# Kernel optimization log

Measured on AMD Instinct MI355X. Metric: run time of the kernel, lower is better.

Reference implementation:

```python
import jax, jax.numpy as jnp
import numpy as np

N_NODES = 100000
N_EDGES = 1600000
N_GRAPHS = 64
IN_C, HID, OUT_C = 9, 128, 2


def setup_inputs() -> dict:
    key = jax.random.key(0)
    ks = jax.random.split(key, 10)
    x = jax.random.normal(ks[0], (N_NODES, IN_C), dtype=jnp.float32)
    edge_index = jax.random.randint(ks[1], (2, N_EDGES), 0, N_NODES, dtype=jnp.int64)
    batch = jnp.sort(jax.random.randint(ks[2], (N_NODES,), 0, N_GRAPHS, dtype=jnp.int64))
    # GCNConv params (glorot-ish scale) and biases
    W1 = jax.random.normal(ks[3], (IN_C, HID), dtype=jnp.float32) / np.sqrt(IN_C)
    b1 = jnp.zeros((HID,), dtype=jnp.float32)
    W2 = jax.random.normal(ks[4], (HID, HID), dtype=jnp.float32) / np.sqrt(HID)
    b2 = jnp.zeros((HID,), dtype=jnp.float32)
    Wc = jax.random.normal(ks[5], (HID, OUT_C), dtype=jnp.float32) / np.sqrt(HID)
    bc = jnp.zeros((OUT_C,), dtype=jnp.float32)
    return {"x": x, "edge_index": edge_index, "batch": batch,
            "W1": W1, "b1": b1, "W2": W2, "b2": b2, "Wc": Wc, "bc": bc}


def _gcn_conv(x, row, col, dinv, W, b):
    # x: [N, Fin] -> [N, Fout]; symmetric-normalized scatter-add over edges+self-loops
    xw = x @ W                                   # dense GEMM
    norm = dinv[row] * dinv[col]                 # [E+N]
    msg = xw[row] * norm[:, None]                # gather + scale
    out = jax.ops.segment_sum(msg, col, num_segments=x.shape[0])  # scatter-add at target
    return out + b


def reference(x, edge_index, batch, W1, b1, W2, b2, Wc, bc):
    n = x.shape[0]
    loops = jnp.arange(n, dtype=edge_index.dtype)
    row = jnp.concatenate([edge_index[0], loops])  # sources (with self-loops)
    col = jnp.concatenate([edge_index[1], loops])  # targets
    deg = jax.ops.segment_sum(jnp.ones_like(col, dtype=x.dtype), col, num_segments=n)
    dinv = jnp.where(deg > 0, jax.lax.rsqrt(deg), 0.0)
    h = jax.nn.relu(_gcn_conv(x, row, col, dinv, W1, b1))
    h = jax.nn.relu(_gcn_conv(h, row, col, dinv, W2, b2))
    # global mean pool over graphs
    sums = jax.ops.segment_sum(h, batch, num_segments=N_GRAPHS)
    cnts = jax.ops.segment_sum(jnp.ones((n,), dtype=h.dtype), batch, num_segments=N_GRAPHS)
    pooled = sums / jnp.maximum(cnts, 1.0)[:, None]
    return pooled @ Wc + bc
```

## Files before the change

### kernel.cpp

```cpp
#include <hip/hip_runtime.h>

#define NN 100000
#define NE 1600000
#define NG 64
#define HIDC 128
#define INC 9
#define OUTC 2
#define BSH 9
#define NBK ((NN + 511) / 512)
#define EPB 4096
#define NBLKA ((NE + EPB - 1) / EPB)
#define CAP 12288

typedef unsigned int u32;

#define PACK_REC(lc, r) (((u32)(lc) << 17) | (u32)(r))
#define REC_LC(v) ((v) >> 17)
#define REC_ROW(v) ((v) & 0x1FFFFu)

__device__ inline float bf_lo(u32 u) { return __uint_as_float(u << 16); }
__device__ inline float bf_hi(u32 u) { return __uint_as_float(u & 0xFFFF0000u); }
__device__ inline u32 f2bf(float x) {
    u32 u = __float_as_uint(x);
    return (u + 0x7FFFu + ((u >> 16) & 1u)) >> 16;
}
__device__ inline u32 packbf(float a, float b) { return f2bf(a) | (f2bf(b) << 16); }

__global__ void k_zero196(int* bcnt) {
    int t = threadIdx.x;
    if (t < NBK) bcnt[t] = 0;
}

__global__ __launch_bounds__(256) void k_bscatter2(const int* __restrict__ row,
                                                   const int* __restrict__ col,
                                                   int* bcnt, u32* __restrict__ staging) {
    __shared__ u32 srec[EPB];
    __shared__ u32 sbkt[EPB];
    __shared__ int hist[NBK];
    __shared__ int base[NBK];
    int t = threadIdx.x;
    long e0 = (long)blockIdx.x * EPB;
    int n = (NE - e0 < EPB) ? (int)(NE - e0) : EPB;
    for (int i = t; i < n; i += 256) {
        u32 c = col[e0 + i];
        u32 r = row[e0 + i];
        srec[i] = PACK_REC(c & 511u, r);
        sbkt[i] = c >> BSH;
    }
    if (t < NBK) hist[t] = 0;
    __syncthreads();
    for (int i = t; i < n; i += 256) atomicAdd(&hist[sbkt[i]], 1);
    __syncthreads();
    if (t < NBK) {
        int h = hist[t];
        base[t] = h ? atomicAdd(&bcnt[t], h) : 0;
        hist[t] = 0;
    }
    __syncthreads();
    for (int i = t; i < n; i += 256) {
        int b = sbkt[i];
        int p = atomicAdd(&hist[b], 1) + base[b];
        if (p < CAP) staging[(long)b * CAP + p] = srec[i];
    }
}

__global__ __launch_bounds__(256) void k_bscan(const int* __restrict__ bcnt,
                                               int* __restrict__ bbase,
                                               int* __restrict__ offsets) {
    __shared__ int lds[256];
    int t = threadIdx.x;
    int v = (t < NBK) ? bcnt[t] : 0;
    lds[t] = v;
    __syncthreads();
    for (int d = 1; d < 256; d <<= 1) {
        int u = (t >= d) ? lds[t - d] : 0;
        __syncthreads();
        lds[t] += u;
        __syncthreads();
    }
    if (t < NBK) bbase[t] = lds[t] - v;
    if (t == 0) offsets[NN] = NE;
}

__global__ __launch_bounds__(256) void k_bcsr(const u32* __restrict__ staging,
                                              const int* __restrict__ bcnt,
                                              const int* __restrict__ bbase,
                                              int* __restrict__ offsets,
                                              float* __restrict__ dinv,
                                              int* __restrict__ csr_src) {
    __shared__ int cnt[512];
    __shared__ int cur[512];
    __shared__ int sc[256];
    int b = blockIdx.x, t = threadIdx.x;
    int nb0 = b << BSH;
    int nodes = NN - nb0 < 512 ? NN - nb0 : 512;
    int ne_b = bcnt[b];
    long s0b = (long)b * CAP;
    int e0 = bbase[b];
    cnt[t] = 0;
    cnt[t + 256] = 0;
    __syncthreads();
    for (int e = t; e < ne_b; e += 256)
        atomicAdd(&cnt[REC_LC(staging[s0b + e])], 1);
    __syncthreads();
    int c0 = cnt[2 * t], c1 = cnt[2 * t + 1];
    int s = c0 + c1;
    sc[t] = s;
    __syncthreads();
    for (int d = 1; d < 256; d <<= 1) {
        int u = (t >= d) ? sc[t - d] : 0;
        __syncthreads();
        sc[t] += u;
        __syncthreads();
    }
    int ex = sc[t] - s;
    cur[2 * t] = ex;
    cur[2 * t + 1] = ex + c0;
    if (2 * t < nodes) {
        offsets[nb0 + 2 * t] = e0 + ex;
        dinv[nb0 + 2 * t] = rsqrtf((float)(c0 + 1));
    }
    if (2 * t + 1 < nodes) {
        offsets[nb0 + 2 * t + 1] = e0 + ex + c0;
        dinv[nb0 + 2 * t + 1] = rsqrtf((float)(c1 + 1));
    }
    __syncthreads();
    for (int e = t; e < ne_b; e += 256) {
        u32 r = staging[s0b + e];
        int p = atomicAdd(&cur[REC_LC(r)], 1);
        csr_src[e0 + p] = (int)REC_ROW(r);
    }
}

__global__ __launch_bounds__(256) void k_xw1(const float* __restrict__ x,
                                             const float* __restrict__ W1,
                                             const float* __restrict__ dinv,
                                             u32* __restrict__ Ap2) {
    int tid = threadIdx.x;
    int i = blockIdx.x * 4 + (tid >> 6);
    int j = tid & 63;
    if (i >= NN) return;
    float acc0 = 0.f, acc1 = 0.f;
#pragma unroll
    for (int k = 0; k < INC; ++k) {
        float xv = x[i * INC + k];
        acc0 += xv * W1[k * HIDC + 2 * j];
        acc1 += xv * W1[k * HIDC + 2 * j + 1];
    }
    float di = dinv[i];
    Ap2[(long)i * 64 + j] = packbf(acc0 * di, acc1 * di);
}

__global__ __launch_bounds__(256) void k_gather(const u32* __restrict__ Ap2,
                                                const int* __restrict__ csr_src,
                                                const int* __restrict__ offsets,
                                                const float* __restrict__ dinv,
                                                u32* __restrict__ B2) {
    int i = (blockIdx.x * 256 + threadIdx.x) >> 6;
    if (i >= NN) return;
    int lane = threadIdx.x & 63;
    long base = (long)i * 64 + lane;
    u32 a = Ap2[base];
    float acc0 = bf_lo(a), acc1 = bf_hi(a);
    int beg = offsets[i], end = offsets[i + 1];
    int e = beg;
    for (; e + 8 <= end; e += 8) {
        int s0 = csr_src[e + 0], s1 = csr_src[e + 1], s2 = csr_src[e + 2], s3 = csr_src[e + 3];
        int s4 = csr_src[e + 4], s5 = csr_src[e + 5], s6 = csr_src[e + 6], s7 = csr_src[e + 7];
        u32 v0 = Ap2[(long)s0 * 64 + lane];
        u32 v1 = Ap2[(long)s1 * 64 + lane];
        u32 v2 = Ap2[(long)s2 * 64 + lane];
        u32 v3 = Ap2[(long)s3 * 64 + lane];
        u32 v4 = Ap2[(long)s4 * 64 + lane];
        u32 v5 = Ap2[(long)s5 * 64 + lane];
        u32 v6 = Ap2[(long)s6 * 64 + lane];
        u32 v7 = Ap2[(long)s7 * 64 + lane];
        acc0 += ((bf_lo(v0) + bf_lo(v1)) + (bf_lo(v2) + bf_lo(v3))) +
                ((bf_lo(v4) + bf_lo(v5)) + (bf_lo(v6) + bf_lo(v7)));
        acc1 += ((bf_hi(v0) + bf_hi(v1)) + (bf_hi(v2) + bf_hi(v3))) +
                ((bf_hi(v4) + bf_hi(v5)) + (bf_hi(v6) + bf_hi(v7)));
    }
    for (; e + 2 <= end; e += 2) {
        int s0 = csr_src[e], s1 = csr_src[e + 1];
        u32 v0 = Ap2[(long)s0 * 64 + lane];
        u32 v1 = Ap2[(long)s1 * 64 + lane];
        acc0 += bf_lo(v0) + bf_lo(v1);
        acc1 += bf_hi(v0) + bf_hi(v1);
    }
    for (; e < end; ++e) {
        u32 v = Ap2[(long)csr_src[e] * 64 + lane];
        acc0 += bf_lo(v);
        acc1 += bf_hi(v);
    }
    float di = dinv[i];
    B2[base] = packbf(acc0 * di, acc1 * di);
}

__global__ __launch_bounds__(256) void k_layer2(const u32* __restrict__ B2,
                                                const float* __restrict__ b1,
                                                const float* __restrict__ W2,
                                                const float* __restrict__ dinv,
                                                u32* __restrict__ Ap2) {
    __shared__ float hs[64][HIDC + 1];
    __shared__ float W2s[32][HIDC];
    int t = threadIdx.x;
    int nb = blockIdx.x * 64;
    int j = t & 63;
    float bb0 = b1[2 * j], bb1 = b1[2 * j + 1];
    for (int n = t >> 6; n < 64; n += 4) {
        int node = nb + n;
        u32 u = (node < NN) ? B2[(long)node * 64 + j] : 0u;
        float h0 = bf_lo(u) + bb0;
        float h1 = bf_hi(u) + bb1;
        hs[n][2 * j] = h0 > 0.f ? h0 : 0.f;
        hs[n][2 * j + 1] = h1 > 0.f ? h1 : 0.f;
    }
    int cg = t & 15, ng = t >> 4;
    int n0 = ng * 4, c0 = cg * 4;
    float acc[4][8] = {};
    for (int kt = 0; kt < 4; ++kt) {
        __syncthreads();
        for (int idx = t; idx < 1024; idx += 256)
            ((float4*)W2s)[idx] = ((const float4*)W2)[kt * 1024 + idx];
        __syncthreads();
#pragma unroll 8
        for (int k = 0; k < 32; ++k) {
            int kk = kt * 32 + k;
            float a0 = hs[n0 + 0][kk], a1 = hs[n0 + 1][kk];
            float a2 = hs[n0 + 2][kk], a3 = hs[n0 + 3][kk];
            float4 w0 = *(const float4*)&W2s[k][c0];
            float4 w1 = *(const float4*)&W2s[k][c0 + 64];
            acc[0][0] += a0 * w0.x; acc[0][1] += a0 * w0.y; acc[0][2] += a0 * w0.z; acc[0][3] += a0 * w0.w;
            acc[0][4] += a0 * w1.x; acc[0][5] += a0 * w1.y; acc[0][6] += a0 * w1.z; acc[0][7] += a0 * w1.w;
            acc[1][0] += a1 * w0.x; acc[1][1] += a1 * w0.y; acc[1][2] += a1 * w0.z; acc[1][3] += a1 * w0.w;
            acc[1][4] += a1 * w1.x; acc[1][5] += a1 * w1.y; acc[1][6] += a1 * w1.z; acc[1][7] += a1 * w1.w;
            acc[2][0] += a2 * w0.x; acc[2][1] += a2 * w0.y; acc[2][2] += a2 * w0.z; acc[2][3] += a2 * w0.w;
            acc[2][4] += a2 * w1.x; acc[2][5] += a2 * w1.y; acc[2][6] += a2 * w1.z; acc[2][7] += a2 * w1.w;
            acc[3][0] += a3 * w0.x; acc[3][1] += a3 * w0.y; acc[3][2] += a3 * w0.z; acc[3][3] += a3 * w0.w;
            acc[3][4] += a3 * w1.x; acc[3][5] += a3 * w1.y; acc[3][6] += a3 * w1.z; acc[3][7] += a3 * w1.w;
        }
    }
#pragma unroll
    for (int r = 0; r < 4; ++r) {
        int node = nb + n0 + r;
        if (node < NN) {
            float di = dinv[node];
            uint2 oa, ob;
            oa.x = packbf(acc[r][0] * di, acc[r][1] * di);
            oa.y = packbf(acc[r][2] * di, acc[r][3] * di);
            ob.x = packbf(acc[r][4] * di, acc[r][5] * di);
            ob.y = packbf(acc[r][6] * di, acc[r][7] * di);
            ((uint2*)Ap2)[(long)node * 32 + cg] = oa;
            ((uint2*)Ap2)[(long)node * 32 + 16 + cg] = ob;
        }
    }
}

__global__ void k_pool_init(float* pooled, float* cnt) {
    int i = blockIdx.x * 256 + threadIdx.x;
    if (i < NG * HIDC) pooled[i] = 0.f;
    if (i < NG) cnt[i] = 0.f;
}

__global__ __launch_bounds__(64) void k_pool(const u32* __restrict__ B2,
                                             const float* __restrict__ b2,
                                             const int* __restrict__ batch,
                                             float* pooled, float* cnt) {
    int f = threadIdx.x;
    int start = blockIdx.x * 64;
    int end = start + 64 < NN ? start + 64 : NN;
    float bb0 = b2[2 * f], bb1 = b2[2 * f + 1];
    float s0 = 0.f, s1 = 0.f;
    int gcur = -1, cl = 0;
    for (int i = start; i < end; ++i) {
        int g = batch[i];
        if (g != gcur) {
            if (gcur >= 0) {
                unsafeAtomicAdd(&pooled[gcur * HIDC + 2 * f], s0);
                unsafeAtomicAdd(&pooled[gcur * HIDC + 2 * f + 1], s1);
                if (f == 0) unsafeAtomicAdd(&cnt[gcur], (float)cl);
            }
            gcur = g; s0 = s1 = 0.f; cl = 0;
        }
        u32 u = B2[(long)i * 64 + f];
        float h0 = bf_lo(u) + bb0;
        float h1 = bf_hi(u) + bb1;
        s0 += h0 > 0.f ? h0 : 0.f;
        s1 += h1 > 0.f ? h1 : 0.f;
        cl++;
    }
    if (gcur >= 0) {
        unsafeAtomicAdd(&pooled[gcur * HIDC + 2 * f], s0);
        unsafeAtomicAdd(&pooled[gcur * HIDC + 2 * f + 1], s1);
        if (f == 0) unsafeAtomicAdd(&cnt[gcur], (float)cl);
    }
}

__global__ __launch_bounds__(128) void k_final(const float* __restrict__ pooled,
                                               const float* __restrict__ cnt,
                                               const float* __restrict__ Wc,
                                               const float* __restrict__ bc,
                                               float* __restrict__ out) {
    __shared__ float v0s[HIDC], v1s[HIDC];
    int g = blockIdx.x, f = threadIdx.x;
    float c = cnt[g]; c = c > 1.f ? c : 1.f;
    float val = pooled[g * HIDC + f] / c;
    v0s[f] = val * Wc[f * OUTC + 0];
    v1s[f] = val * Wc[f * OUTC + 1];
    __syncthreads();
    if (f < 2) {
        const float* arr = (f == 0) ? v0s : v1s;
        float s = 0.f;
        for (int k = 0; k < HIDC; ++k) s += arr[k];
        out[g * OUTC + f] = s + bc[f];
    }
}

extern "C" void kernel_launch(void* const* d_in, const int* in_sizes, int n_in,
                              void* d_out, int out_size, void* d_ws, size_t ws_size,
                              hipStream_t stream) {
    const float* x     = (const float*)d_in[0];
    const int*   ei    = (const int*)d_in[1];
    const int*   batch = (const int*)d_in[2];
    const float* W1    = (const float*)d_in[3];
    const float* b1    = (const float*)d_in[4];
    const float* W2    = (const float*)d_in[5];
    const float* b2    = (const float*)d_in[6];
    const float* Wc    = (const float*)d_in[7];
    const float* bc    = (const float*)d_in[8];
    float* out = (float*)d_out;

    char* ws = (char*)d_ws;
    size_t off = 0;
    auto alloc = [&](size_t bytes) { void* p = ws + off; off += (bytes + 255) / 256 * 256; return p; };
    u32*   Ap2     = (u32*)alloc((size_t)NN * 64 * 4);
    u32*   B2      = (u32*)alloc((size_t)NN * 64 * 4);
    float* dinv    = (float*)alloc((size_t)NN * 4);
    int*   offsets = (int*)alloc((size_t)(NN + 1) * 4);
    int*   csr_src = (int*)alloc((size_t)NE * 4);
    u32*   staging = (u32*)alloc((size_t)NBK * CAP * 4);
    int*   bcnt    = (int*)alloc((size_t)NBK * 4);
    int*   bbase   = (int*)alloc((size_t)NBK * 4);
    float* pooled  = (float*)alloc((size_t)NG * HIDC * 4);
    float* cnt     = (float*)alloc((size_t)NG * 4);

    const int* row = ei;
    const int* col = ei + NE;

    k_zero196<<<1, 256, 0, stream>>>(bcnt);
    k_bscatter2<<<NBLKA, 256, 0, stream>>>(row, col, bcnt, staging);
    k_bscan<<<1, 256, 0, stream>>>(bcnt, bbase, offsets);
    k_bcsr<<<NBK, 256, 0, stream>>>(staging, bcnt, bbase, offsets, dinv, csr_src);

    k_xw1<<<(NN + 3) / 4, 256, 0, stream>>>(x, W1, dinv, Ap2);
    k_gather<<<(NN * 64 + 255) / 256, 256, 0, stream>>>(Ap2, csr_src, offsets, dinv, B2);

    k_layer2<<<(NN + 63) / 64, 256, 0, stream>>>(B2, b1, W2, dinv, Ap2);
    k_gather<<<(NN * 64 + 255) / 256, 256, 0, stream>>>(Ap2, csr_src, offsets, dinv, B2);

    k_pool_init<<<(NG * HIDC + 255) / 256, 256, 0, stream>>>(pooled, cnt);
    k_pool<<<(NN + 63) / 64, 64, 0, stream>>>(B2, b2, batch, pooled, cnt);
    k_final<<<NG, 128, 0, stream>>>(pooled, cnt, Wc, bc, out);
}
```

Baseline: 311.3 us.

## Split gather into feature slices with edge-parallel lanes and shuffle reduction

The CSR gather kernel is restructured so each block handles one 8-column slice of the feature row for 32 nodes. Each wave walks 8 nodes in turn, with its 64 lanes split into 8 edge-ways by 8 features, and the partial sums are combined with a shuffle reduction. The aim is more memory-level parallelism per node and slice-major block ordering, so that blocks working on the same feature columns can share cache. In exchange, each gathered row segment is only 32 bytes, csr_src is re-read once per slice (8 times in total), and the csr_src loads and B2 stores are marked nontemporal.

```diff
diff --git a/kernel.cpp b/kernel.cpp
--- a/kernel.cpp
+++ b/kernel.cpp
@@ -156,44 +156,43 @@
                                                 const int* __restrict__ offsets,
                                                 const float* __restrict__ dinv,
                                                 u32* __restrict__ B2) {
-    int i = (blockIdx.x * 256 + threadIdx.x) >> 6;
-    if (i >= NN) return;
-    int lane = threadIdx.x & 63;
-    long base = (long)i * 64 + lane;
-    u32 a = Ap2[base];
-    float acc0 = bf_lo(a), acc1 = bf_hi(a);
-    int beg = offsets[i], end = offsets[i + 1];
-    int e = beg;
-    for (; e + 8 <= end; e += 8) {
-        int s0 = csr_src[e + 0], s1 = csr_src[e + 1], s2 = csr_src[e + 2], s3 = csr_src[e + 3];
-        int s4 = csr_src[e + 4], s5 = csr_src[e + 5], s6 = csr_src[e + 6], s7 = csr_src[e + 7];
-        u32 v0 = Ap2[(long)s0 * 64 + lane];
-        u32 v1 = Ap2[(long)s1 * 64 + lane];
-        u32 v2 = Ap2[(long)s2 * 64 + lane];
-        u32 v3 = Ap2[(long)s3 * 64 + lane];
-        u32 v4 = Ap2[(long)s4 * 64 + lane];
-        u32 v5 = Ap2[(long)s5 * 64 + lane];
-        u32 v6 = Ap2[(long)s6 * 64 + lane];
-        u32 v7 = Ap2[(long)s7 * 64 + lane];
-        acc0 += ((bf_lo(v0) + bf_lo(v1)) + (bf_lo(v2) + bf_lo(v3))) +
-                ((bf_lo(v4) + bf_lo(v5)) + (bf_lo(v6) + bf_lo(v7)));
-        acc1 += ((bf_hi(v0) + bf_hi(v1)) + (bf_hi(v2) + bf_hi(v3))) +
-                ((bf_hi(v4) + bf_hi(v5)) + (bf_hi(v6) + bf_hi(v7)));
-    }
-    for (; e + 2 <= end; e += 2) {
-        int s0 = csr_src[e], s1 = csr_src[e + 1];
-        u32 v0 = Ap2[(long)s0 * 64 + lane];
-        u32 v1 = Ap2[(long)s1 * 64 + lane];
-        acc0 += bf_lo(v0) + bf_lo(v1);
-        acc1 += bf_hi(v0) + bf_hi(v1);
-    }
-    for (; e < end; ++e) {
-        u32 v = Ap2[(long)csr_src[e] * 64 + lane];
-        acc0 += bf_lo(v);
-        acc1 += bf_hi(v);
-    }
-    float di = dinv[i];
-    B2[base] = packbf(acc0 * di, acc1 * di);
+    int slice = blockIdx.x & 7;
+    int chunk = blockIdx.x >> 3;
+    int wv = threadIdx.x >> 6, lane = threadIdx.x & 63;
+    int way = lane >> 3, feat = lane & 7;
+    int fcol = slice * 8 + feat;
+    int i0 = chunk * 32 + wv * 8;
+#pragma unroll 1
+    for (int n = 0; n < 8; ++n) {
+        int i = i0 + n;
+        if (i >= NN) break;
+        int beg = offsets[i], end = offsets[i + 1];
+        float acc0 = 0.f, acc1 = 0.f;
+        int e = beg + way;
+        for (; e + 8 < end; e += 16) {
+            int s0 = __builtin_nontemporal_load(&csr_src[e]);
+            int s1 = __builtin_nontemporal_load(&csr_src[e + 8]);
+            u32 v0 = Ap2[(long)s0 * 64 + fcol];
+            u32 v1 = Ap2[(long)s1 * 64 + fcol];
+            acc0 += bf_lo(v0) + bf_lo(v1);
+            acc1 += bf_hi(v0) + bf_hi(v1);
+        }
+        if (e < end) {
+            int s = __builtin_nontemporal_load(&csr_src[e]);
+            u32 v = Ap2[(long)s * 64 + fcol];
+            acc0 += bf_lo(v);
+            acc1 += bf_hi(v);
+        }
+        acc0 += __shfl_down(acc0, 32); acc1 += __shfl_down(acc1, 32);
+        acc0 += __shfl_down(acc0, 16); acc1 += __shfl_down(acc1, 16);
+        acc0 += __shfl_down(acc0, 8);  acc1 += __shfl_down(acc1, 8);
+        if (way == 0) {
+            u32 a = Ap2[(long)i * 64 + fcol];
+            float di = dinv[i];
+            u32 o = packbf((acc0 + bf_lo(a)) * di, (acc1 + bf_hi(a)) * di);
+            __builtin_nontemporal_store(o, &B2[(long)i * 64 + fcol]);
+        }
+    }
 }
 
 __global__ __launch_bounds__(256) void k_layer2(const u32* __restrict__ B2,
@@ -352,11 +351,13 @@
     k_bscan<<<1, 256, 0, stream>>>(bcnt, bbase, offsets);
     k_bcsr<<<NBK, 256, 0, stream>>>(staging, bcnt, bbase, offsets, dinv, csr_src);
 
+    const int GATHER_BLKS = 8 * ((NN + 31) / 32);
+
     k_xw1<<<(NN + 3) / 4, 256, 0, stream>>>(x, W1, dinv, Ap2);
-    k_gather<<<(NN * 64 + 255) / 256, 256, 0, stream>>>(Ap2, csr_src, offsets, dinv, B2);
+    k_gather<<<GATHER_BLKS, 256, 0, stream>>>(Ap2, csr_src, offsets, dinv, B2);
 
     k_layer2<<<(NN + 63) / 64, 256, 0, stream>>>(B2, b1, W2, dinv, Ap2);
-    k_gather<<<(NN * 64 + 255) / 256, 256, 0, stream>>>(Ap2, csr_src, offsets, dinv, B2);
+    k_gather<<<GATHER_BLKS, 256, 0, stream>>>(Ap2, csr_src, offsets, dinv, B2);
 
     k_pool_init<<<(NG * HIDC + 255) / 256, 256, 0, stream>>>(pooled, cnt);
     k_pool<<<(NN + 63) / 64, 64, 0, stream>>>(B2, b2, batch, pooled, cnt);
```

New measurement: 864.2 us. +177.6%, slower.

## Retile layer-2 GEMM to 128 nodes per block with transposed bf16 LDS staging

Applied to the files above, without the earlier changes.

The layer-2 dense GEMM now handles 128 nodes per block instead of 64. Each thread accumulates an 8x8 tile rather than 4x8. Post-ReLU activations are stored in shared memory as a transposed bf16-pair array, so each thread reads 8 nodes' values for two k indices with two 128-bit loads. Input loads are widened to uint4, and the zeroing kernel is replaced by hipMemsetAsync. The aim is fewer LDS reads per FMA and less W2 reloading per node, at the cost of more registers (64 accumulators) and possibly lower occupancy.

```diff
diff --git a/kernel.cpp b/kernel.cpp
--- a/kernel.cpp
+++ b/kernel.cpp
@@ -25,11 +25,6 @@
     return (u + 0x7FFFu + ((u >> 16) & 1u)) >> 16;
 }
 __device__ inline u32 packbf(float a, float b) { return f2bf(a) | (f2bf(b) << 16); }
-
-__global__ void k_zero196(int* bcnt) {
-    int t = threadIdx.x;
-    if (t < NBK) bcnt[t] = 0;
-}
 
 __global__ __launch_bounds__(256) void k_bscatter2(const int* __restrict__ row,
                                                    const int* __restrict__ col,
@@ -201,47 +196,65 @@
                                                 const float* __restrict__ W2,
                                                 const float* __restrict__ dinv,
                                                 u32* __restrict__ Ap2) {
-    __shared__ float hs[64][HIDC + 1];
+    __shared__ u32 hsT[64][132];
     __shared__ float W2s[32][HIDC];
     int t = threadIdx.x;
-    int nb = blockIdx.x * 64;
-    int j = t & 63;
-    float bb0 = b1[2 * j], bb1 = b1[2 * j + 1];
-    for (int n = t >> 6; n < 64; n += 4) {
-        int node = nb + n;
-        u32 u = (node < NN) ? B2[(long)node * 64 + j] : 0u;
-        float h0 = bf_lo(u) + bb0;
-        float h1 = bf_hi(u) + bb1;
-        hs[n][2 * j] = h0 > 0.f ? h0 : 0.f;
-        hs[n][2 * j + 1] = h1 > 0.f ? h1 : 0.f;
-    }
+    int nb = blockIdx.x * 128;
+    long base64 = (long)nb * 64;
+
+    int j0 = 4 * (t & 15);
+    float4 bA = *(const float4*)&b1[2 * j0];
+    float4 bB = *(const float4*)&b1[2 * j0 + 4];
+#pragma unroll
+    for (int c = 0; c < 8; ++c) {
+        int nl = c * 16 + (t >> 4);
+        uint4 u = (nb + nl < NN) ? *(const uint4*)&B2[base64 + (long)nl * 64 + j0]
+                                 : make_uint4(0, 0, 0, 0);
+        float h0, h1;
+        h0 = bf_lo(u.x) + bA.x; h1 = bf_hi(u.x) + bA.y;
+        hsT[j0 + 0][nl] = packbf(h0 > 0.f ? h0 : 0.f, h1 > 0.f ? h1 : 0.f);
+        h0 = bf_lo(u.y) + bA.z; h1 = bf_hi(u.y) + bA.w;
+        hsT[j0 + 1][nl] = packbf(h0 > 0.f ? h0 : 0.f, h1 > 0.f ? h1 : 0.f);
+        h0 = bf_lo(u.z) + bB.x; h1 = bf_hi(u.z) + bB.y;
+        hsT[j0 + 2][nl] = packbf(h0 > 0.f ? h0 : 0.f, h1 > 0.f ? h1 : 0.f);
+        h0 = bf_lo(u.w) + bB.z; h1 = bf_hi(u.w) + bB.w;
+        hsT[j0 + 3][nl] = packbf(h0 > 0.f ? h0 : 0.f, h1 > 0.f ? h1 : 0.f);
+    }
+
     int cg = t & 15, ng = t >> 4;
-    int n0 = ng * 4, c0 = cg * 4;
-    float acc[4][8] = {};
+    int n0 = ng * 8, c0 = cg * 4;
+    float acc[8][8] = {};
     for (int kt = 0; kt < 4; ++kt) {
         __syncthreads();
         for (int idx = t; idx < 1024; idx += 256)
             ((float4*)W2s)[idx] = ((const float4*)W2)[kt * 1024 + idx];
         __syncthreads();
-#pragma unroll 8
-        for (int k = 0; k < 32; ++k) {
-            int kk = kt * 32 + k;
-            float a0 = hs[n0 + 0][kk], a1 = hs[n0 + 1][kk];
-            float a2 = hs[n0 + 2][kk], a3 = hs[n0 + 3][kk];
-            float4 w0 = *(const float4*)&W2s[k][c0];
-            float4 w1 = *(const float4*)&W2s[k][c0 + 64];
-            acc[0][0] += a0 * w0.x; acc[0][1] += a0 * w0.y; acc[0][2] += a0 * w0.z; acc[0][3] += a0 * w0.w;
-            acc[0][4] += a0 * w1.x; acc[0][5] += a0 * w1.y; acc[0][6] += a0 * w1.z; acc[0][7] += a0 * w1.w;
-            acc[1][0] += a1 * w0.x; acc[1][1] += a1 * w0.y; acc[1][2] += a1 * w0.z; acc[1][3] += a1 * w0.w;
-            acc[1][4] += a1 * w1.x; acc[1][5] += a1 * w1.y; acc[1][6] += a1 * w1.z; acc[1][7] += a1 * w1.w;
-            acc[2][0] += a2 * w0.x; acc[2][1] += a2 * w0.y; acc[2][2] += a2 * w0.z; acc[2][3] += a2 * w0.w;
-            acc[2][4] += a2 * w1.x; acc[2][5] += a2 * w1.y; acc[2][6] += a2 * w1.z; acc[2][7] += a2 * w1.w;
-            acc[3][0] += a3 * w0.x; acc[3][1] += a3 * w0.y; acc[3][2] += a3 * w0.z; acc[3][3] += a3 * w0.w;
-            acc[3][4] += a3 * w1.x; acc[3][5] += a3 * w1.y; acc[3][6] += a3 * w1.z; acc[3][7] += a3 * w1.w;
+#pragma unroll
+        for (int kp = 0; kp < 16; ++kp) {
+            int kpi = kt * 16 + kp;
+            uint4 ha = *(const uint4*)&hsT[kpi][n0];
+            uint4 hb = *(const uint4*)&hsT[kpi][n0 + 4];
+            float4 we0 = *(const float4*)&W2s[2 * kp][c0];
+            float4 we1 = *(const float4*)&W2s[2 * kp][c0 + 64];
+            float4 wo0 = *(const float4*)&W2s[2 * kp + 1][c0];
+            float4 wo1 = *(const float4*)&W2s[2 * kp + 1][c0 + 64];
+            u32 hu[8] = {ha.x, ha.y, ha.z, ha.w, hb.x, hb.y, hb.z, hb.w};
+#pragma unroll
+            for (int r = 0; r < 8; ++r) {
+                float ae = bf_lo(hu[r]), ao = bf_hi(hu[r]);
+                acc[r][0] += ae * we0.x + ao * wo0.x;
+                acc[r][1] += ae * we0.y + ao * wo0.y;
+                acc[r][2] += ae * we0.z + ao * wo0.z;
+                acc[r][3] += ae * we0.w + ao * wo0.w;
+                acc[r][4] += ae * we1.x + ao * wo1.x;
+                acc[r][5] += ae * we1.y + ao * wo1.y;
+                acc[r][6] += ae * we1.z + ao * wo1.z;
+                acc[r][7] += ae * we1.w + ao * wo1.w;
+            }
         }
     }
 #pragma unroll
-    for (int r = 0; r < 4; ++r) {
+    for (int r = 0; r < 8; ++r) {
         int node = nb + n0 + r;
         if (node < NN) {
             float di = dinv[node];
@@ -347,7 +360,7 @@
     const int* row = ei;
     const int* col = ei + NE;
 
-    k_zero196<<<1, 256, 0, stream>>>(bcnt);
+    hipMemsetAsync(bcnt, 0, (size_t)NBK * 4, stream);
     k_bscatter2<<<NBLKA, 256, 0, stream>>>(row, col, bcnt, staging);
     k_bscan<<<1, 256, 0, stream>>>(bcnt, bbase, offsets);
     k_bcsr<<<NBK, 256, 0, stream>>>(staging, bcnt, bbase, offsets, dinv, csr_src);
@@ -355,7 +368,7 @@
     k_xw1<<<(NN + 3) / 4, 256, 0, stream>>>(x, W1, dinv, Ap2);
     k_gather<<<(NN * 64 + 255) / 256, 256, 0, stream>>>(Ap2, csr_src, offsets, dinv, B2);
 
-    k_layer2<<<(NN + 63) / 64, 256, 0, stream>>>(B2, b1, W2, dinv, Ap2);
+    k_layer2<<<(NN + 127) / 128, 256, 0, stream>>>(B2, b1, W2, dinv, Ap2);
     k_gather<<<(NN * 64 + 255) / 256, 256, 0, stream>>>(Ap2, csr_src, offsets, dinv, B2);
 
     k_pool_init<<<(NG * HIDC + 255) / 256, 256, 0, stream>>>(pooled, cnt);
```

Result: slower. 406.6 us (+30.6%).
